# Kernel optimization log

Hardware: AMD Instinct MI355X
Metric: run time of the kernel (lower is better)

Reference implementation:

```python
import jax, jax.numpy as jnp
import numpy as np

D = 32
B = 4096
T = 256
HIDDEN = 64
DT = 0.005


def setup_inputs() -> dict:
    key = jax.random.key(0)
    ks = jax.random.split(key, 6)
    s1 = 1.0 / np.sqrt(D + 1)
    s2 = 1.0 / np.sqrt(HIDDEN)
    return {
        "z0": jax.random.normal(ks[0], (B, D), dtype=jnp.float32),
        "ts": jnp.arange(T, dtype=jnp.float32) * DT,
        "noise": jax.random.normal(ks[1], (T - 1, B, D), dtype=jnp.float32),
        "W1": jax.random.normal(ks[2], (D + 1, HIDDEN), dtype=jnp.float32) * s1,
        "b1": jnp.zeros((HIDDEN,), dtype=jnp.float32),
        "W2": jax.random.normal(ks[3], (HIDDEN, HIDDEN), dtype=jnp.float32) * s2,
        "b2": jnp.zeros((HIDDEN,), dtype=jnp.float32),
        "W3": jax.random.normal(ks[4], (HIDDEN, D), dtype=jnp.float32) * s2,
        "b3": jnp.zeros((D,), dtype=jnp.float32),
        "log_std": jnp.full((D,), -1.0, dtype=jnp.float32),
    }


def reference(z0, ts, noise, W1, b1, W2, b2, W3, b3, log_std):
    """Euler-Maruyama integration of the posterior SDE.

    dz = f_phi(t, z) dt + diag(exp(log_std)) dW,  dW = sqrt(dt) * noise.
    Returns ys of shape [T, B, D] with ys[0] = z0 (matches torchsde.sdeint).
    """
    std = jnp.exp(log_std)  # [D], constant diagonal diffusion
    dts = ts[1:] - ts[:-1]  # [T-1]

    def drift(t, y):
        # MLP on cat([t, y]): Linear -> tanh -> Linear -> tanh -> Linear
        tt = jnp.broadcast_to(t, (y.shape[0], 1)).astype(y.dtype)
        h = jnp.tanh(jnp.concatenate([tt, y], axis=-1) @ W1 + b1)
        h = jnp.tanh(h @ W2 + b2)
        return h @ W3 + b3  # [B, D]

    def step(y, xs):
        t, dt, dw = xs
        y_next = y + drift(t, y) * dt + std * jnp.sqrt(dt) * dw
        return y_next, y_next

    _, ys = jax.lax.scan(step, z0, (ts[:-1], dts, noise))
    return jnp.concatenate([z0[None], ys], axis=0)  # [T, B, D]
```

## Files before the change

### kernel.cpp

```cpp
#include <hip/hip_runtime.h>

#define NB 4096
#define NT 256
#define DTC 0.005f
#define SQDT 0.07071067811865475f
#define KS 1024.0f
#define NRM (1.0f / 65535.0f)

typedef __bf16 bf16x8 __attribute__((ext_vector_type(8)));
typedef float f32x4 __attribute__((ext_vector_type(4)));
typedef unsigned int u32;
typedef unsigned int u32x4 __attribute__((ext_vector_type(4)));
typedef unsigned short u16;
typedef u16 u16x2 __attribute__((ext_vector_type(2)));

static __device__ __forceinline__ f32x4 mfma16(bf16x8 a, bf16x8 b, f32x4 c) {
  return __builtin_amdgcn_mfma_f32_16x16x32_bf16(a, b, c, 0, 0, 0);
}

static __device__ __forceinline__ u32 act2(const char* lb, u32 clampv,
                                           float a, float b) {
  u32 p, q;
  asm("v_cvt_pknorm_u16_f32 %0, %1, %2" : "=v"(p) : "v"(a), "v"(b));
  asm("v_pk_min_u16 %0, %1, %2" : "=v"(q) : "v"(p), "v"(clampv));
  q &= 0xFFFEFFFEu;
  u16x2 pr;
  pr.x = *reinterpret_cast<const u16*>(lb + (q & 0xFFFFu));
  pr.y = *reinterpret_cast<const u16*>(lb + (q >> 16));
  return __builtin_bit_cast(u32, pr);
}

static __device__ __forceinline__ bf16x8 mkfrag(u32 a, u32 b, u32 c, u32 d) {
  u32x4 v;
  v[0] = a; v[1] = b; v[2] = c; v[3] = d;
  return __builtin_bit_cast(bf16x8, v);
}

__global__ __launch_bounds__(64) void sde_kernel(
    const float* __restrict__ z0, const float* __restrict__ ts,
    const float* __restrict__ noise, const float* __restrict__ W1,
    const float* __restrict__ b1, const float* __restrict__ W2,
    const float* __restrict__ b2, const float* __restrict__ W3,
    const float* __restrict__ b3, const float* __restrict__ log_std,
    float* __restrict__ out) {
  (void)ts;
  __shared__ u16 lut[4096];

  const int lane = threadIdx.x;
  const int c = lane & 15;
  const int g = lane >> 4;
  const int R = blockIdx.x * 16 + c;

  for (int i = lane; i < 4096; i += 64) {
    float x = (float)(i - 2048) * (1.0f / 512.0f);
    float e = __builtin_amdgcn_exp2f(x * 2.885390082f);
    float t = __builtin_fmaf(-2.0f, __builtin_amdgcn_rcpf(e + 1.0f), 1.0f);
    __bf16 tb = (__bf16)t;
    lut[i] = __builtin_bit_cast(u16, tb);
  }
  asm volatile("s_waitcnt lgkmcnt(0)" ::: "memory");
  const char* lb = reinterpret_cast<const char*>(lut);
  const u32 clampv = 0x1FFE1FFEu;

  int sig[8];
#pragma unroll
  for (int j = 0; j < 8; ++j) sig[j] = 16 * (j >> 2) + 4 * g + (j & 3);

  bf16x8 a1s[4], a2f[4][2], a3f[2][2];
#pragma unroll
  for (int ot = 0; ot < 4; ++ot)
#pragma unroll
    for (int j = 0; j < 8; ++j)
      a1s[ot][j] = (__bf16)(KS * NRM * W1[(1 + sig[j]) * 64 + 16 * ot + c]);
#pragma unroll
  for (int ot = 0; ot < 4; ++ot)
#pragma unroll
    for (int kf = 0; kf < 2; ++kf)
#pragma unroll
      for (int j = 0; j < 8; ++j)
        a2f[ot][kf][j] =
            (__bf16)(KS * NRM * W2[(32 * kf + sig[j]) * 64 + 16 * ot + c]);
#pragma unroll
  for (int ot = 0; ot < 2; ++ot)
#pragma unroll
    for (int kf = 0; kf < 2; ++kf)
#pragma unroll
      for (int j = 0; j < 8; ++j)
        a3f[ot][kf][j] = (__bf16)W3[(32 * kf + sig[j]) * 32 + 16 * ot + c];

  f32x4 c1i[4], dcq[4], d2C[4];
#pragma unroll
  for (int ot = 0; ot < 4; ++ot)
#pragma unroll
    for (int r = 0; r < 4; ++r) {
      int d = 16 * ot + 4 * g + r;
      c1i[ot][r] = (__builtin_fmaf(KS, b1[d], 4096.0f)) * NRM;
      dcq[ot][r] = KS * NRM * DTC * W1[d];
      d2C[ot][r] = (__builtin_fmaf(KS, b2[d], 4096.0f)) * NRM;
    }
  f32x4 b3v[2], ssd[2];
#pragma unroll
  for (int ot = 0; ot < 2; ++ot)
#pragma unroll
    for (int r = 0; r < 4; ++r) {
      int d = 16 * ot + 4 * g + r;
      b3v[ot][r] = b3[d];
      ssd[ot][r] = expf(log_std[d]) * SQDT;
    }

  f32x4 y0v = *reinterpret_cast<const f32x4*>(z0 + (size_t)R * 32 + 4 * g);
  f32x4 y1v = *reinterpret_cast<const f32x4*>(z0 + (size_t)R * 32 + 16 + 4 * g);
  *reinterpret_cast<f32x4*>(out + (size_t)R * 32 + 4 * g) = y0v;
  *reinterpret_cast<f32x4*>(out + (size_t)R * 32 + 16 + 4 * g) = y1v;

  bf16x8 yb;
#pragma unroll
  for (int j = 0; j < 8; ++j)
    yb[j] = (__bf16)((j >> 2) ? y1v[j & 3] : y0v[j & 3]);

  const float* nzp0 = noise + ((size_t)0 * NB + R) * 32 + 4 * g;
  f32x4 nzA0 = *reinterpret_cast<const f32x4*>(nzp0);
  f32x4 nzA1 = *reinterpret_cast<const f32x4*>(nzp0 + 16);
  const float* nzp1 = noise + ((size_t)1 * NB + R) * 32 + 4 * g;
  f32x4 nzB0 = *reinterpret_cast<const f32x4*>(nzp1);
  f32x4 nzB1 = *reinterpret_cast<const f32x4*>(nzp1 + 16);

  float* outP = out + (size_t)(NB + R) * 32 + 4 * g;
  const size_t ostep = (size_t)NB * 32;

  auto STEP = [&](int t, f32x4& nu0, f32x4& nu1) {
    int tn = t + 2;
    tn = tn > NT - 2 ? NT - 2 : tn;
    const float* nzp = noise + ((size_t)tn * NB + R) * 32 + 4 * g;
    f32x4 pf0 = *reinterpret_cast<const f32x4*>(nzp);
    f32x4 pf1 = *reinterpret_cast<const f32x4*>(nzp + 16);

    float tq = (float)t;

    f32x4 d1[4];
#pragma unroll
    for (int ot = 0; ot < 4; ++ot) {
      f32x4 ci;
#pragma unroll
      for (int r = 0; r < 4; ++r)
        ci[r] = __builtin_fmaf(tq, dcq[ot][r], c1i[ot][r]);
      d1[ot] = mfma16(a1s[ot], yb, ci);
    }
    bf16x8 h1b0 = mkfrag(act2(lb, clampv, d1[0][0], d1[0][1]),
                         act2(lb, clampv, d1[0][2], d1[0][3]),
                         act2(lb, clampv, d1[1][0], d1[1][1]),
                         act2(lb, clampv, d1[1][2], d1[1][3]));
    bf16x8 h1b1 = mkfrag(act2(lb, clampv, d1[2][0], d1[2][1]),
                         act2(lb, clampv, d1[2][2], d1[2][3]),
                         act2(lb, clampv, d1[3][0], d1[3][1]),
                         act2(lb, clampv, d1[3][2], d1[3][3]));

    f32x4 d2[4];
#pragma unroll
    for (int ot = 0; ot < 4; ++ot)
      d2[ot] = mfma16(a2f[ot][1], h1b1, mfma16(a2f[ot][0], h1b0, d2C[ot]));
    bf16x8 h2b0 = mkfrag(act2(lb, clampv, d2[0][0], d2[0][1]),
                         act2(lb, clampv, d2[0][2], d2[0][3]),
                         act2(lb, clampv, d2[1][0], d2[1][1]),
                         act2(lb, clampv, d2[1][2], d2[1][3]));
    bf16x8 h2b1 = mkfrag(act2(lb, clampv, d2[2][0], d2[2][1]),
                         act2(lb, clampv, d2[2][2], d2[2][3]),
                         act2(lb, clampv, d2[3][0], d2[3][1]),
                         act2(lb, clampv, d2[3][2], d2[3][3]));

    f32x4 l30 = mfma16(a3f[0][1], h2b1, mfma16(a3f[0][0], h2b0, b3v[0]));
    f32x4 l31 = mfma16(a3f[1][1], h2b1, mfma16(a3f[1][0], h2b0, b3v[1]));

    y0v = y0v + l30 * DTC + ssd[0] * nu0;
    y1v = y1v + l31 * DTC + ssd[1] * nu1;
    *reinterpret_cast<f32x4*>(outP) = y0v;
    *reinterpret_cast<f32x4*>(outP + 16) = y1v;
    outP += ostep;

#pragma unroll
    for (int j = 0; j < 8; ++j)
      yb[j] = (__bf16)((j >> 2) ? y1v[j & 3] : y0v[j & 3]);

    nu0 = pf0;
    nu1 = pf1;
  };

  for (int t = 0; t < NT - 2; t += 2) {
    STEP(t, nzA0, nzA1);
    STEP(t + 1, nzB0, nzB1);
  }
  STEP(NT - 2, nzA0, nzA1);
}

extern "C" void kernel_launch(void* const* d_in, const int* in_sizes, int n_in,
                              void* d_out, int out_size, void* d_ws, size_t ws_size,
                              hipStream_t stream) {
  (void)in_sizes; (void)n_in; (void)out_size; (void)d_ws; (void)ws_size;
  const float* z0   = (const float*)d_in[0];
  const float* ts   = (const float*)d_in[1];
  const float* nz   = (const float*)d_in[2];
  const float* W1   = (const float*)d_in[3];
  const float* b1   = (const float*)d_in[4];
  const float* W2   = (const float*)d_in[5];
  const float* b2   = (const float*)d_in[6];
  const float* W3   = (const float*)d_in[7];
  const float* b3   = (const float*)d_in[8];
  const float* lstd = (const float*)d_in[9];
  float* out = (float*)d_out;
  hipLaunchKernelGGL(sde_kernel, dim3(NB / 16), dim3(64), 0, stream,
                     z0, ts, nz, W1, b1, W2, b2, W3, b3, lstd, out);
}
```

Before: 157.7 us.

## Split K-dim MFMA chains and overlap with activation lookups, use packed bf16 cvt

Splits each two-MFMA dependent accumulation chain into two independent MFMAs plus a vector add. The first-half MFMAs can then issue while the second half of the activation LUT lookups is still running, shortening the serial critical path of each timestep. It also replaces the per-element bf16 conversion with packed v_cvt_pk_bf16_f32, turns the time-dependent bias into an incremental add, and replaces prefetch index arithmetic with a pointer stride. The extra f32 adds and the changed accumulation order add a little VALU work and may slightly change rounding.

```diff
diff --git a/kernel.cpp b/kernel.cpp
--- a/kernel.cpp
+++ b/kernel.cpp
@@ -36,6 +36,12 @@
   return __builtin_bit_cast(bf16x8, v);
 }
 
+static __device__ __forceinline__ u32 pkbf(float a, float b) {
+  u32 r;
+  asm("v_cvt_pk_bf16_f32 %0, %1, %2" : "=v"(r) : "v"(a), "v"(b));
+  return r;
+}
+
 __global__ __launch_bounds__(64) void sde_kernel(
     const float* __restrict__ z0, const float* __restrict__ ts,
     const float* __restrict__ noise, const float* __restrict__ W1,
@@ -88,13 +94,13 @@
       for (int j = 0; j < 8; ++j)
         a3f[ot][kf][j] = (__bf16)W3[(32 * kf + sig[j]) * 32 + 16 * ot + c];
 
-  f32x4 c1i[4], dcq[4], d2C[4];
+  f32x4 ci[4], dcq[4], d2C[4];
 #pragma unroll
   for (int ot = 0; ot < 4; ++ot)
 #pragma unroll
     for (int r = 0; r < 4; ++r) {
       int d = 16 * ot + 4 * g + r;
-      c1i[ot][r] = (__builtin_fmaf(KS, b1[d], 4096.0f)) * NRM;
+      ci[ot][r] = (__builtin_fmaf(KS, b1[d], 4096.0f)) * NRM;
       dcq[ot][r] = KS * NRM * DTC * W1[d];
       d2C[ot][r] = (__builtin_fmaf(KS, b2[d], 4096.0f)) * NRM;
     }
@@ -107,79 +113,78 @@
       b3v[ot][r] = b3[d];
       ssd[ot][r] = expf(log_std[d]) * SQDT;
     }
+  const f32x4 zero4 = {0.f, 0.f, 0.f, 0.f};
 
   f32x4 y0v = *reinterpret_cast<const f32x4*>(z0 + (size_t)R * 32 + 4 * g);
   f32x4 y1v = *reinterpret_cast<const f32x4*>(z0 + (size_t)R * 32 + 16 + 4 * g);
   *reinterpret_cast<f32x4*>(out + (size_t)R * 32 + 4 * g) = y0v;
   *reinterpret_cast<f32x4*>(out + (size_t)R * 32 + 16 + 4 * g) = y1v;
 
-  bf16x8 yb;
-#pragma unroll
-  for (int j = 0; j < 8; ++j)
-    yb[j] = (__bf16)((j >> 2) ? y1v[j & 3] : y0v[j & 3]);
-
-  const float* nzp0 = noise + ((size_t)0 * NB + R) * 32 + 4 * g;
-  f32x4 nzA0 = *reinterpret_cast<const f32x4*>(nzp0);
-  f32x4 nzA1 = *reinterpret_cast<const f32x4*>(nzp0 + 16);
-  const float* nzp1 = noise + ((size_t)1 * NB + R) * 32 + 4 * g;
-  f32x4 nzB0 = *reinterpret_cast<const f32x4*>(nzp1);
-  f32x4 nzB1 = *reinterpret_cast<const f32x4*>(nzp1 + 16);
-
-  float* outP = out + (size_t)(NB + R) * 32 + 4 * g;
-  const size_t ostep = (size_t)NB * 32;
+  bf16x8 yb = mkfrag(pkbf(y0v[0], y0v[1]), pkbf(y0v[2], y0v[3]),
+                     pkbf(y1v[0], y1v[1]), pkbf(y1v[2], y1v[3]));
+
+  const size_t nstride = (size_t)NB * 32 * sizeof(float);
+  const char* nzbase = (const char*)(noise + ((size_t)R * 32 + 4 * g));
+  f32x4 nzA0 = *(const f32x4*)(nzbase);
+  f32x4 nzA1 = *(const f32x4*)(nzbase + 64);
+  f32x4 nzB0 = *(const f32x4*)(nzbase + nstride);
+  f32x4 nzB1 = *(const f32x4*)(nzbase + nstride + 64);
+  const char* pfp = nzbase + 2 * nstride;
+
+  char* outP = (char*)(out + ((size_t)NB + R) * 32 + 4 * g);
 
   auto STEP = [&](int t, f32x4& nu0, f32x4& nu1) {
-    int tn = t + 2;
-    tn = tn > NT - 2 ? NT - 2 : tn;
-    const float* nzp = noise + ((size_t)tn * NB + R) * 32 + 4 * g;
-    f32x4 pf0 = *reinterpret_cast<const f32x4*>(nzp);
-    f32x4 pf1 = *reinterpret_cast<const f32x4*>(nzp + 16);
-
-    float tq = (float)t;
+    f32x4 pf0 = *(const f32x4*)(pfp);
+    f32x4 pf1 = *(const f32x4*)(pfp + 64);
+    if (t < NT - 4) pfp += nstride;
 
     f32x4 d1[4];
 #pragma unroll
-    for (int ot = 0; ot < 4; ++ot) {
-      f32x4 ci;
-#pragma unroll
-      for (int r = 0; r < 4; ++r)
-        ci[r] = __builtin_fmaf(tq, dcq[ot][r], c1i[ot][r]);
-      d1[ot] = mfma16(a1s[ot], yb, ci);
-    }
+    for (int ot = 0; ot < 4; ++ot) d1[ot] = mfma16(a1s[ot], yb, ci[ot]);
+#pragma unroll
+    for (int ot = 0; ot < 4; ++ot) ci[ot] = ci[ot] + dcq[ot];
+
     bf16x8 h1b0 = mkfrag(act2(lb, clampv, d1[0][0], d1[0][1]),
                          act2(lb, clampv, d1[0][2], d1[0][3]),
                          act2(lb, clampv, d1[1][0], d1[1][1]),
                          act2(lb, clampv, d1[1][2], d1[1][3]));
+    f32x4 pa[4];
+#pragma unroll
+    for (int ot = 0; ot < 4; ++ot) pa[ot] = mfma16(a2f[ot][0], h1b0, d2C[ot]);
     bf16x8 h1b1 = mkfrag(act2(lb, clampv, d1[2][0], d1[2][1]),
                          act2(lb, clampv, d1[2][2], d1[2][3]),
                          act2(lb, clampv, d1[3][0], d1[3][1]),
                          act2(lb, clampv, d1[3][2], d1[3][3]));
-
+    f32x4 pb[4];
+#pragma unroll
+    for (int ot = 0; ot < 4; ++ot) pb[ot] = mfma16(a2f[ot][1], h1b1, zero4);
     f32x4 d2[4];
 #pragma unroll
-    for (int ot = 0; ot < 4; ++ot)
-      d2[ot] = mfma16(a2f[ot][1], h1b1, mfma16(a2f[ot][0], h1b0, d2C[ot]));
+    for (int ot = 0; ot < 4; ++ot) d2[ot] = pa[ot] + pb[ot];
+
     bf16x8 h2b0 = mkfrag(act2(lb, clampv, d2[0][0], d2[0][1]),
                          act2(lb, clampv, d2[0][2], d2[0][3]),
                          act2(lb, clampv, d2[1][0], d2[1][1]),
                          act2(lb, clampv, d2[1][2], d2[1][3]));
+    f32x4 qa0 = mfma16(a3f[0][0], h2b0, b3v[0]);
+    f32x4 qa1 = mfma16(a3f[1][0], h2b0, b3v[1]);
     bf16x8 h2b1 = mkfrag(act2(lb, clampv, d2[2][0], d2[2][1]),
                          act2(lb, clampv, d2[2][2], d2[2][3]),
                          act2(lb, clampv, d2[3][0], d2[3][1]),
                          act2(lb, clampv, d2[3][2], d2[3][3]));
-
-    f32x4 l30 = mfma16(a3f[0][1], h2b1, mfma16(a3f[0][0], h2b0, b3v[0]));
-    f32x4 l31 = mfma16(a3f[1][1], h2b1, mfma16(a3f[1][0], h2b0, b3v[1]));
-
+    f32x4 qb0 = mfma16(a3f[0][1], h2b1, zero4);
+    f32x4 qb1 = mfma16(a3f[1][1], h2b1, zero4);
+
+    f32x4 l30 = qa0 + qb0;
+    f32x4 l31 = qa1 + qb1;
     y0v = y0v + l30 * DTC + ssd[0] * nu0;
     y1v = y1v + l31 * DTC + ssd[1] * nu1;
-    *reinterpret_cast<f32x4*>(outP) = y0v;
-    *reinterpret_cast<f32x4*>(outP + 16) = y1v;
-    outP += ostep;
-
-#pragma unroll
-    for (int j = 0; j < 8; ++j)
-      yb[j] = (__bf16)((j >> 2) ? y1v[j & 3] : y0v[j & 3]);
+    *(f32x4*)(outP) = y0v;
+    *(f32x4*)(outP + 64) = y1v;
+    outP += nstride;
+
+    yb = mkfrag(pkbf(y0v[0], y0v[1]), pkbf(y0v[2], y0v[3]),
+                pkbf(y1v[0], y1v[1]), pkbf(y1v[2], y1v[3]));
 
     nu0 = pf0;
     nu1 = pf1;
```

Result: slower. 272.5 us (+72.7%).
